# Kernel tuning notes

Hardware: AMD Instinct MI355X
Metric: run time of the kernel (lower is better)

## Reference

```python
import jax, jax.numpy as jnp
import numpy as np
from jax import lax

# SLAYER neuron / simulation constants (netParams)
THETA = 1.0      # spike threshold
TAU_SR = 4.0     # PSP (SRM) kernel time constant
TAU_REF = 1.0    # refractory kernel time constant
SCALE_REF = 2.0  # refractory scale (kernel amplitude = -scaleRef*theta)
TAU_RHO = 1.0    # surrogate-gradient width (used in bwd only)
SCALE_RHO = 1.0

B, F_IN, T = 8, 6300, 500  # 6300 = 50*63*2
HID, OUT = 32, 20


def _alpha_scan(x, d):
    """Causal conv with alpha kernel k*d**k along last (time) axis via 2-state recurrence.
    x: [..., T]. y[t] = sum_{j<=t} x[j]*(t-j)*d**(t-j)."""
    xt = jnp.moveaxis(x, -1, 0)  # [T, ...]
    zero = jnp.zeros_like(xt[0])

    def step(carry, xi):
        z, y = carry
        y_new = d * (y + z)       # y[t] = d*(y[t-1] + z[t-1])
        z_new = d * z + xi        # z[t] = d*z[t-1] + x[t]
        return (z_new, y_new), y_new

    _, ys = lax.scan(step, (zero, zero), xt)
    return jnp.moveaxis(ys, 0, -1)


def psp(x):
    """SLAYER psp: convolve spike train with SRM kernel eps(k) = (k/tauSr)*exp(1-k/tauSr)."""
    d = float(np.exp(-1.0 / TAU_SR))
    return jnp.float32(np.e / TAU_SR) * _alpha_scan(x, d)


def _spike_impl(p):
    """Iterative threshold + refractory. p: [..., T] membrane input (post-psp, post-dense).
    Refractory kernel: ref(k) = -scaleRef*theta*(k/tauRef)*exp(1-k/tauRef), realized by the
    same 2-state alpha recurrence driven by emitted spikes."""
    d = float(np.exp(-1.0 / TAU_REF))
    C = jnp.float32(-SCALE_REF * THETA * np.e / TAU_REF)
    pt = jnp.moveaxis(p, -1, 0)  # [T, ...]
    zero = jnp.zeros_like(pt[0])

    def step(carry, pi):
        z, y = carry
        y_new = d * (y + z)                 # alpha state from past spikes (lag>=1)
        u = pi + C * y_new                  # membrane potential incl. refractory
        s = (u >= THETA).astype(pi.dtype)   # hard threshold
        z_new = d * z + s
        return (z_new, y_new), s

    _, ss = lax.scan(step, (zero, zero), pt)
    return jnp.moveaxis(ss, 0, -1)


def spike(p):
    return _spike_impl(p)


def setup_inputs() -> dict:
    key = jax.random.key(0)
    k1, k2, k3 = jax.random.split(key, 3)
    downsampled = (jax.random.uniform(k1, (B, F_IN, T)) < 0.05).astype(jnp.float32)
    w1 = jax.random.normal(k2, (HID, F_IN), jnp.float32) * 0.05
    w2 = jax.random.normal(k3, (OUT, HID), jnp.float32) * 0.3
    return {"downsampled": downsampled, "w1": w1, "w2": w2}


def reference(downsampled, w1, w2):
    # spike_1 = spike(psp(downsampled))
    s1 = spike(psp(downsampled))
    # spike_2 = spike(fc1(psp(spike_1)))
    s2 = spike(jnp.einsum('of,bft->bot', w1, psp(s1)))
    # spike_3 = spike(fc2(psp(spike_2)))
    s3 = spike(jnp.einsum('of,bft->bot', w2, psp(s2)))
    return s3
```

## Files before the change

kernel.cpp:

```cpp
#include <hip/hip_runtime.h>
#include <stdint.h>

#define NB 8
#define F_IN 6300
#define NT 500
#define HID 32
#define NOUT 20
#define NW 99

#define D_SR   0.7788007830714049f
#define S_SR   0.6795704571147613f
#define D_REF  0.36787944117144233f
#define C_REF  -5.43656365691809f

__global__ __launch_bounds__(256) void k0_transpose(const float* __restrict__ w1,
                                                    double* __restrict__ w1td) {
  __shared__ float tl[64][33];
  const int f0 = blockIdx.x * 64;
  const int tid = threadIdx.x;
  const int r = tid & 63, g = tid >> 6;
#pragma unroll
  for (int oo = 0; oo < 32; oo += 4) {
    int o = oo + g;
    int f = f0 + r;
    tl[r][o] = (f < F_IN) ? w1[o * F_IN + f] : 0.f;
  }
  __syncthreads();
#pragma unroll
  for (int k = 0; k < 8; k++) {
    int idx = k * 256 + tid;
    int rr = idx >> 5, cc = idx & 31;
    int f = f0 + rr;
    if (f < F_IN) w1td[(size_t)f * 32 + cc] = (double)tl[rr][cc];
  }
}

#define CH_T 100

__global__ __launch_bounds__(64) void k1_layer1(const float* __restrict__ x,
                                                uint64_t* __restrict__ masks) {
  __shared__ float tile[CH_T][65];
  const int wi = blockIdx.x;
  const int b  = blockIdx.y;
  const int lane = threadIdx.x;
  const int f = wi * 64 + lane;
  const float vm = (f < F_IN) ? 1.0f : 0.0f;
  const float* xblk = x + (size_t)b * F_IN * NT;
  uint64_t* mrow = masks + ((size_t)b * NW + wi) * NT;

  int goff[25], fidv[25], jv[25];
#pragma unroll
  for (int k = 0; k < 25; k++) {
    int idx = k * 64 + lane;
    int fid = idx / 25;
    int j = idx - fid * 25;
    int rf = wi * 64 + fid;
    if (rf >= F_IN) rf = F_IN - 1;
    goff[k] = rf * NT + 4 * j;
    fidv[k] = fid;
    jv[k] = j;
  }

  float z1 = 0.f, y1 = 0.f, zr = 0.f, yr = 0.f;
  float4 ld[25];
#pragma unroll
  for (int k = 0; k < 25; k++) ld[k] = *(const float4*)(xblk + goff[k]);

  for (int c = 0; c < 5; c++) {
#pragma unroll
    for (int k = 0; k < 25; k++) {
      int r = 4 * jv[k], fd = fidv[k];
      tile[r + 0][fd] = ld[k].x;
      tile[r + 1][fd] = ld[k].y;
      tile[r + 2][fd] = ld[k].z;
      tile[r + 3][fd] = ld[k].w;
    }
    if (c + 1 < 5) {
      const float* gb = xblk + (c + 1) * CH_T;
#pragma unroll
      for (int k = 0; k < 25; k++) ld[k] = *(const float4*)(gb + goff[k]);
    }
    uint64_t keep0 = 0, keep1 = 0;
#pragma unroll
    for (int tc = 0; tc < CH_T; tc++) {
      float xi = tile[tc][lane] * vm;
      y1 = __fmul_rn(D_SR, __fadd_rn(y1, z1));
      z1 = __fadd_rn(__fmul_rn(D_SR, z1), xi);
      float p = __fmul_rn(S_SR, y1);
      yr = __fmul_rn(D_REF, __fadd_rn(yr, zr));
      float u = __fadd_rn(p, __fmul_rn(C_REF, yr));
      bool s = (u >= 1.0f);
      zr = __fadd_rn(__fmul_rn(D_REF, zr), s ? 1.0f : 0.0f);
      uint64_t m = __ballot(s);
      if (tc < 64) { if (lane == tc)      keep0 = m; }
      else         { if (lane == tc - 64) keep1 = m; }
    }
    uint64_t* mp = mrow + c * CH_T;
    mp[lane] = keep0;
    if (lane < CH_T - 64) mp[64 + lane] = keep1;
  }
}

__global__ __launch_bounds__(256) void k2_fc1(const double* __restrict__ w1td,
                                              const uint64_t* __restrict__ masks,
                                              double* __restrict__ R) {
  const int lane = threadIdx.x & 63;
  const int wave = threadIdx.x >> 6;
  const int half = lane >> 5;
  const int o = lane & 31;
  const int b = blockIdx.x;
  const int t = blockIdx.y * 4 + wave;
  const uint64_t* mbase = masks + (size_t)b * NW * NT + t;
  const char* wbase = (const char*)w1td + o * 8;
  double acc = 0.0;
  uint64_t mcur = mbase[(size_t)half * NT];
  for (int wi = half; wi < NW; wi += 2) {
    uint64_t mnext = (wi + 2 < NW) ? mbase[(size_t)(wi + 2) * NT] : 0;
    uint32_t lo = (uint32_t)mcur;
    uint32_t hi = (uint32_t)(mcur >> 32);
    uint32_t off0 = (uint32_t)wi * (64 * 256);
    while (lo) {
      int i = __builtin_ctz(lo);
      lo &= lo - 1;
      acc += *(const double*)(wbase + off0 + ((uint32_t)i << 8));
    }
    uint32_t off1 = off0 + 32 * 256;
    while (hi) {
      int i = __builtin_ctz(hi);
      hi &= hi - 1;
      acc += *(const double*)(wbase + off1 + ((uint32_t)i << 8));
    }
    mcur = mnext;
  }
  int hi2 = __shfl_xor(__double2hiint(acc), 32);
  int lo2 = __shfl_xor(__double2loint(acc), 32);
  acc += __hiloint2double(hi2, lo2);
  if (half == 0) R[((size_t)b * HID + o) * NT + t] = acc;
}

__device__ __forceinline__ bool snn_step(double ri, double& z2, double& y2,
                                         double& zr, double& yr) {
  const double dsr = (double)D_SR, ssr = (double)S_SR;
  const double dre = (double)D_REF, cr = (double)C_REF;
  y2 = dsr * (y2 + z2);
  z2 = dsr * z2 + ri;
  double p = ssr * y2;
  yr = dre * (yr + zr);
  double u = p + cr * yr;
  bool s = (u >= 1.0);
  zr = dre * zr + (s ? 1.0 : 0.0);
  return s;
}

__global__ __launch_bounds__(64) void k3_spike2(const double* __restrict__ R,
                                                uint8_t* __restrict__ s2) {
  int id = blockIdx.x * 64 + threadIdx.x;
  int b = id >> 5, h = id & 31;
  const double2* r2 = (const double2*)(R + (size_t)id * NT);
  uint8_t* sp = s2 + (size_t)b * NT * HID + h;
  double z2 = 0, y2 = 0, zr = 0, yr = 0;
  double2 g0a = r2[0], g0b = r2[1];
  double2 g1a = r2[2], g1b = r2[3];
  double2 g2a = r2[4], g2b = r2[5];
  double2 g3a = r2[6], g3b = r2[7];
  for (int g = 0; g < 125; g++) {
    sp[0]       = snn_step(g0a.x, z2, y2, zr, yr) ? 1 : 0;
    sp[HID]     = snn_step(g0a.y, z2, y2, zr, yr) ? 1 : 0;
    sp[2 * HID] = snn_step(g0b.x, z2, y2, zr, yr) ? 1 : 0;
    sp[3 * HID] = snn_step(g0b.y, z2, y2, zr, yr) ? 1 : 0;
    sp += 4 * HID;
    g0a = g1a; g0b = g1b; g1a = g2a; g1b = g2b; g2a = g3a; g2b = g3b;
    if (g + 4 < 125) { g3a = r2[(g + 4) * 2]; g3b = r2[(g + 4) * 2 + 1]; }
  }
}

__global__ __launch_bounds__(256) void k4_fc2(const float* __restrict__ w2,
                                              const uint8_t* __restrict__ s2,
                                              double* __restrict__ R3) {
  int id = blockIdx.x * 256 + threadIdx.x;
  if (id >= NB * NOUT * NT) return;
  int t = id % NT;
  int bo = id / NT;
  int o = bo % NOUT;
  int b = bo / NOUT;
  const uint8_t* row = s2 + (size_t)(b * NT + t) * HID;
  const float* wr = w2 + o * HID;
  double acc = 0.0;
#pragma unroll
  for (int h = 0; h < HID; h += 4) {
    uint32_t m = *(const uint32_t*)(row + h);
    float4 w = *(const float4*)(wr + h);
    if (m & 0x000000FFu) acc += (double)w.x;
    if (m & 0x0000FF00u) acc += (double)w.y;
    if (m & 0x00FF0000u) acc += (double)w.z;
    if (m & 0xFF000000u) acc += (double)w.w;
  }
  R3[(size_t)bo * NT + t] = acc;
}

__global__ __launch_bounds__(64) void k5_out(const double* __restrict__ R3,
                                             float* __restrict__ out) {
  int id = blockIdx.x * 64 + threadIdx.x;
  if (id >= NB * NOUT) return;
  const double2* r2 = (const double2*)(R3 + (size_t)id * NT);
  float* orow = out + (size_t)id * NT;
  double z2 = 0, y2 = 0, zr = 0, yr = 0;
  double2 g0a = r2[0], g0b = r2[1];
  double2 g1a = r2[2], g1b = r2[3];
  double2 g2a = r2[4], g2b = r2[5];
  double2 g3a = r2[6], g3b = r2[7];
  for (int g = 0; g < 125; g++) {
    orow[0] = snn_step(g0a.x, z2, y2, zr, yr) ? 1.0f : 0.0f;
    orow[1] = snn_step(g0a.y, z2, y2, zr, yr) ? 1.0f : 0.0f;
    orow[2] = snn_step(g0b.x, z2, y2, zr, yr) ? 1.0f : 0.0f;
    orow[3] = snn_step(g0b.y, z2, y2, zr, yr) ? 1.0f : 0.0f;
    orow += 4;
    g0a = g1a; g0b = g1b; g1a = g2a; g1b = g2b; g2a = g3a; g2b = g3b;
    if (g + 4 < 125) { g3a = r2[(g + 4) * 2]; g3b = r2[(g + 4) * 2 + 1]; }
  }
}

extern "C" void kernel_launch(void* const* d_in, const int* in_sizes, int n_in,
                              void* d_out, int out_size, void* d_ws, size_t ws_size,
                              hipStream_t stream) {
  const float* x  = (const float*)d_in[0];
  const float* w1 = (const float*)d_in[1];
  const float* w2 = (const float*)d_in[2];
  float* out = (float*)d_out;

  uint8_t* ws = (uint8_t*)d_ws;
  const size_t W1TD_BYTES = (size_t)F_IN * HID * 8;
  const size_t MASK_BYTES = (size_t)NB * NW * NT * 8;
  const size_t R_BYTES    = (size_t)NB * HID * NT * 8;
  const size_t S2_BYTES   = (size_t)NB * NT * HID;
  double*   w1td  = (double*)ws;
  uint64_t* masks = (uint64_t*)(ws + W1TD_BYTES);
  double*   R     = (double*)(ws + W1TD_BYTES + MASK_BYTES);
  uint8_t*  s2    = ws + W1TD_BYTES + MASK_BYTES + R_BYTES;
  double*   R3    = (double*)(ws + W1TD_BYTES + MASK_BYTES + R_BYTES + S2_BYTES);

  k0_transpose<<<99, 256, 0, stream>>>(w1, w1td);
  k1_layer1<<<dim3(NW, NB), 64, 0, stream>>>(x, masks);
  k2_fc1<<<dim3(NB, NT / 4), 256, 0, stream>>>(w1td, masks, R);
  k3_spike2<<<4, 64, 0, stream>>>(R, s2);
  k4_fc2<<<(NB * NOUT * NT + 255) / 256, 256, 0, stream>>>(w2, s2, R3);
  k5_out<<<3, 64, 0, stream>>>(R3, out);
}
```

Before: 334.8 us.

## Fuse spike2, fc2 and output spike kernels; split fc1 over wave segments

Merges the layer-2 spike scan, fc2 and output spike scan into one per-batch kernel that keeps spike masks, w2 and fc2 results in shared memory instead of global buffers. fc1 now stores transposed w1 as float instead of double, which halves the gather traffic. Its block doubles to 512 threads so two wave groups each handle half the mask words, and it unrolls the bit-scan four indices at a time for more memory-level parallelism. The costs are an extra shared-memory reduction and a serial 500-step output scan run by only 20 threads per block.

```diff
diff --git a/kernel.cpp b/kernel.cpp
--- a/kernel.cpp
+++ b/kernel.cpp
@@ -14,7 +14,7 @@
 #define C_REF  -5.43656365691809f
 
 __global__ __launch_bounds__(256) void k0_transpose(const float* __restrict__ w1,
-                                                    double* __restrict__ w1td) {
+                                                    float* __restrict__ w1t) {
   __shared__ float tl[64][33];
   const int f0 = blockIdx.x * 64;
   const int tid = threadIdx.x;
@@ -31,7 +31,7 @@
     int idx = k * 256 + tid;
     int rr = idx >> 5, cc = idx & 31;
     int f = f0 + rr;
-    if (f < F_IN) w1td[(size_t)f * 32 + cc] = (double)tl[rr][cc];
+    if (f < F_IN) w1t[(size_t)f * 32 + cc] = tl[rr][cc];
   }
 }
 
@@ -101,41 +101,63 @@
   }
 }
 
-__global__ __launch_bounds__(256) void k2_fc1(const double* __restrict__ w1td,
+__global__ __launch_bounds__(512) void k2_fc1(const float* __restrict__ w1t,
                                               const uint64_t* __restrict__ masks,
                                               double* __restrict__ R) {
-  const int lane = threadIdx.x & 63;
-  const int wave = threadIdx.x >> 6;
+  __shared__ double part[8][32];
+  const int tid = threadIdx.x;
+  const int wv = tid >> 6;
+  const int lane = tid & 63;
   const int half = lane >> 5;
   const int o = lane & 31;
   const int b = blockIdx.x;
-  const int t = blockIdx.y * 4 + wave;
+  const int t = blockIdx.y * 4 + (wv & 3);
+  const int seg = wv >> 2;
+  const int wbeg = seg * 50, wend = seg ? NW : 50;
   const uint64_t* mbase = masks + (size_t)b * NW * NT + t;
-  const char* wbase = (const char*)w1td + o * 8;
+  const char* wrow = (const char*)w1t + o * 4;
   double acc = 0.0;
-  uint64_t mcur = mbase[(size_t)half * NT];
-  for (int wi = half; wi < NW; wi += 2) {
-    uint64_t mnext = (wi + 2 < NW) ? mbase[(size_t)(wi + 2) * NT] : 0;
-    uint32_t lo = (uint32_t)mcur;
-    uint32_t hi = (uint32_t)(mcur >> 32);
-    uint32_t off0 = (uint32_t)wi * (64 * 256);
-    while (lo) {
-      int i = __builtin_ctz(lo);
-      lo &= lo - 1;
-      acc += *(const double*)(wbase + off0 + ((uint32_t)i << 8));
-    }
-    uint32_t off1 = off0 + 32 * 256;
-    while (hi) {
-      int i = __builtin_ctz(hi);
-      hi &= hi - 1;
-      acc += *(const double*)(wbase + off1 + ((uint32_t)i << 8));
+
+  int wi = wbeg + half;
+  uint64_t mcur = (wi < wend) ? mbase[(size_t)wi * NT] : 0;
+  for (; wi < wend; wi += 2) {
+    uint64_t mnext = (wi + 2 < wend) ? mbase[(size_t)(wi + 2) * NT] : 0;
+    const uint32_t base0 = ((uint32_t)wi << 13);
+    uint32_t w = (uint32_t)mcur;
+    uint32_t boff = base0;
+#pragma unroll
+    for (int sub = 0; sub < 2; sub++) {
+      while (w) {
+        uint32_t i0 = __builtin_ctz(w);                 uint32_t w1_ = w & (w - 1);
+        uint32_t i1 = w1_ ? __builtin_ctz(w1_) : 0u;    uint32_t w2_ = w1_ ? (w1_ & (w1_ - 1)) : 0u;
+        uint32_t i2 = w2_ ? __builtin_ctz(w2_) : 0u;    uint32_t w3_ = w2_ ? (w2_ & (w2_ - 1)) : 0u;
+        uint32_t i3 = w3_ ? __builtin_ctz(w3_) : 0u;    w = w3_ ? (w3_ & (w3_ - 1)) : 0u;
+        float a0 = *(const float*)(wrow + boff + (i0 << 7));
+        float a1 = *(const float*)(wrow + boff + (i1 << 7));
+        float a2 = *(const float*)(wrow + boff + (i2 << 7));
+        float a3 = *(const float*)(wrow + boff + (i3 << 7));
+        a1 = w1_ ? a1 : 0.0f;
+        a2 = w2_ ? a2 : 0.0f;
+        a3 = w3_ ? a3 : 0.0f;
+        acc += (double)a0;
+        acc += (double)a1;
+        acc += (double)a2;
+        acc += (double)a3;
+      }
+      w = (uint32_t)(mcur >> 32);
+      boff = base0 + (32u << 7);
     }
     mcur = mnext;
   }
   int hi2 = __shfl_xor(__double2hiint(acc), 32);
   int lo2 = __shfl_xor(__double2loint(acc), 32);
   acc += __hiloint2double(hi2, lo2);
-  if (half == 0) R[((size_t)b * HID + o) * NT + t] = acc;
+  if (half == 0) part[wv][o] = acc;
+  __syncthreads();
+  if (wv < 4 && half == 0) {
+    double tot = part[wv][o] + part[wv + 4][o];
+    R[((size_t)b * HID + o) * NT + t] = tot;
+  }
 }
 
 __device__ __forceinline__ bool snn_step(double ri, double& z2, double& y2,
@@ -152,71 +174,72 @@
   return s;
 }
 
-__global__ __launch_bounds__(64) void k3_spike2(const double* __restrict__ R,
-                                                uint8_t* __restrict__ s2) {
-  int id = blockIdx.x * 64 + threadIdx.x;
-  int b = id >> 5, h = id & 31;
-  const double2* r2 = (const double2*)(R + (size_t)id * NT);
-  uint8_t* sp = s2 + (size_t)b * NT * HID + h;
-  double z2 = 0, y2 = 0, zr = 0, yr = 0;
-  double2 g0a = r2[0], g0b = r2[1];
-  double2 g1a = r2[2], g1b = r2[3];
-  double2 g2a = r2[4], g2b = r2[5];
-  double2 g3a = r2[6], g3b = r2[7];
-  for (int g = 0; g < 125; g++) {
-    sp[0]       = snn_step(g0a.x, z2, y2, zr, yr) ? 1 : 0;
-    sp[HID]     = snn_step(g0a.y, z2, y2, zr, yr) ? 1 : 0;
-    sp[2 * HID] = snn_step(g0b.x, z2, y2, zr, yr) ? 1 : 0;
-    sp[3 * HID] = snn_step(g0b.y, z2, y2, zr, yr) ? 1 : 0;
-    sp += 4 * HID;
-    g0a = g1a; g0b = g1b; g1a = g2a; g1b = g2b; g2a = g3a; g2b = g3b;
-    if (g + 4 < 125) { g3a = r2[(g + 4) * 2]; g3b = r2[(g + 4) * 2 + 1]; }
-  }
-}
-
-__global__ __launch_bounds__(256) void k4_fc2(const float* __restrict__ w2,
-                                              const uint8_t* __restrict__ s2,
-                                              double* __restrict__ R3) {
-  int id = blockIdx.x * 256 + threadIdx.x;
-  if (id >= NB * NOUT * NT) return;
-  int t = id % NT;
-  int bo = id / NT;
-  int o = bo % NOUT;
-  int b = bo / NOUT;
-  const uint8_t* row = s2 + (size_t)(b * NT + t) * HID;
-  const float* wr = w2 + o * HID;
-  double acc = 0.0;
-#pragma unroll
-  for (int h = 0; h < HID; h += 4) {
-    uint32_t m = *(const uint32_t*)(row + h);
-    float4 w = *(const float4*)(wr + h);
-    if (m & 0x000000FFu) acc += (double)w.x;
-    if (m & 0x0000FF00u) acc += (double)w.y;
-    if (m & 0x00FF0000u) acc += (double)w.z;
-    if (m & 0xFF000000u) acc += (double)w.w;
-  }
-  R3[(size_t)bo * NT + t] = acc;
-}
-
-__global__ __launch_bounds__(64) void k5_out(const double* __restrict__ R3,
-                                             float* __restrict__ out) {
-  int id = blockIdx.x * 64 + threadIdx.x;
-  if (id >= NB * NOUT) return;
-  const double2* r2 = (const double2*)(R3 + (size_t)id * NT);
-  float* orow = out + (size_t)id * NT;
-  double z2 = 0, y2 = 0, zr = 0, yr = 0;
-  double2 g0a = r2[0], g0b = r2[1];
-  double2 g1a = r2[2], g1b = r2[3];
-  double2 g2a = r2[4], g2b = r2[5];
-  double2 g3a = r2[6], g3b = r2[7];
-  for (int g = 0; g < 125; g++) {
-    orow[0] = snn_step(g0a.x, z2, y2, zr, yr) ? 1.0f : 0.0f;
-    orow[1] = snn_step(g0a.y, z2, y2, zr, yr) ? 1.0f : 0.0f;
-    orow[2] = snn_step(g0b.x, z2, y2, zr, yr) ? 1.0f : 0.0f;
-    orow[3] = snn_step(g0b.y, z2, y2, zr, yr) ? 1.0f : 0.0f;
-    orow += 4;
-    g0a = g1a; g0b = g1b; g1a = g2a; g1b = g2b; g2a = g3a; g2b = g3b;
-    if (g + 4 < 125) { g3a = r2[(g + 4) * 2]; g3b = r2[(g + 4) * 2 + 1]; }
+__global__ __launch_bounds__(256) void k345(const double* __restrict__ R,
+                                            const float* __restrict__ w2,
+                                            float* __restrict__ out) {
+  __shared__ uint32_t s2m[NT];
+  __shared__ float    w2l[NOUT][33];
+  __shared__ double   r3[NT][NOUT];
+  const int tid = threadIdx.x;
+  const int b = blockIdx.x;
+
+  if (tid >= 64) {
+    for (int i = tid - 64; i < NOUT * HID; i += 192)
+      w2l[i >> 5][i & 31] = w2[i];
+  } else {
+    const int lane = tid;
+    const int h = lane & 31;
+    const bool act = lane < HID;
+    const double2* r2 = (const double2*)(R + ((size_t)b * HID + h) * NT);
+    double z2 = 0, y2 = 0, zr = 0, yr = 0;
+    double2 g0a = r2[0], g0b = r2[1];
+    double2 g1a = r2[2], g1b = r2[3];
+    double2 g2a = r2[4], g2b = r2[5];
+    double2 g3a = r2[6], g3b = r2[7];
+    for (int g = 0; g < 125; g++) {
+      const int t = g * 4;
+      double v0 = act ? g0a.x : 0.0, v1 = act ? g0a.y : 0.0;
+      double v2 = act ? g0b.x : 0.0, v3 = act ? g0b.y : 0.0;
+      uint64_t m0 = __ballot(snn_step(v0, z2, y2, zr, yr) && act);
+      uint64_t m1 = __ballot(snn_step(v1, z2, y2, zr, yr) && act);
+      uint64_t m2 = __ballot(snn_step(v2, z2, y2, zr, yr) && act);
+      uint64_t m3 = __ballot(snn_step(v3, z2, y2, zr, yr) && act);
+      if (lane == 0) {
+        s2m[t + 0] = (uint32_t)m0;
+        s2m[t + 1] = (uint32_t)m1;
+        s2m[t + 2] = (uint32_t)m2;
+        s2m[t + 3] = (uint32_t)m3;
+      }
+      g0a = g1a; g0b = g1b; g1a = g2a; g1b = g2b; g2a = g3a; g2b = g3b;
+      if (g + 4 < 125) { g3a = r2[(g + 4) * 2]; g3b = r2[(g + 4) * 2 + 1]; }
+    }
+  }
+  __syncthreads();
+
+  if (tid < 240) {
+    const int o = tid / 12;
+    const int sl = tid % 12;
+    for (int t = sl; t < NT; t += 12) {
+      uint32_t m = s2m[t];
+      double acc = 0.0;
+      while (m) {
+        int i = __builtin_ctz(m);
+        m &= m - 1;
+        acc += (double)w2l[o][i];
+      }
+      r3[t][o] = acc;
+    }
+  }
+  __syncthreads();
+
+  if (tid < NOUT) {
+    const int o = tid;
+    float* orow = out + ((size_t)b * NOUT + o) * NT;
+    double z2 = 0, y2 = 0, zr = 0, yr = 0;
+    for (int t = 0; t < NT; t++) {
+      bool s = snn_step(r3[t][o], z2, y2, zr, yr);
+      orow[t] = s ? 1.0f : 0.0f;
+    }
   }
 }
 
@@ -229,20 +252,14 @@
   float* out = (float*)d_out;
 
   uint8_t* ws = (uint8_t*)d_ws;
-  const size_t W1TD_BYTES = (size_t)F_IN * HID * 8;
+  const size_t W1T_BYTES  = (size_t)F_IN * HID * 4;
   const size_t MASK_BYTES = (size_t)NB * NW * NT * 8;
-  const size_t R_BYTES    = (size_t)NB * HID * NT * 8;
-  const size_t S2_BYTES   = (size_t)NB * NT * HID;
-  double*   w1td  = (double*)ws;
-  uint64_t* masks = (uint64_t*)(ws + W1TD_BYTES);
-  double*   R     = (double*)(ws + W1TD_BYTES + MASK_BYTES);
-  uint8_t*  s2    = ws + W1TD_BYTES + MASK_BYTES + R_BYTES;
-  double*   R3    = (double*)(ws + W1TD_BYTES + MASK_BYTES + R_BYTES + S2_BYTES);
-
-  k0_transpose<<<99, 256, 0, stream>>>(w1, w1td);
+  float*    w1t   = (float*)ws;
+  uint64_t* masks = (uint64_t*)(ws + W1T_BYTES);
+  double*   R     = (double*)(ws + W1T_BYTES + MASK_BYTES);
+
+  k0_transpose<<<99, 256, 0, stream>>>(w1, w1t);
   k1_layer1<<<dim3(NW, NB), 64, 0, stream>>>(x, masks);
-  k2_fc1<<<dim3(NB, NT / 4), 256, 0, stream>>>(w1td, masks, R);
-  k3_spike2<<<4, 64, 0, stream>>>(R, s2);
-  k4_fc2<<<(NB * NOUT * NT + 255) / 256, 256, 0, stream>>>(w2, s2, R3);
-  k5_out<<<3, 64, 0, stream>>>(R3, out);
-}
+  k2_fc1<<<dim3(NB, NT / 4), 512, 0, stream>>>(w1t, masks, R);
+  k345<<<NB, 256, 0, stream>>>(R, w2, out);
+}
```

Result: faster. 316.2 us (-5.6%).
